# Kernel optimization log

Measured on AMD Instinct MI355X. Metric: run time of the kernel, lower is better.

The kernel has to match this reference:

```python
import jax, jax.numpy as jnp
import numpy as np

D_MODEL = 512
D_PROJ = 32
N_CENT = 6
CORR_HIDDEN = max(D_MODEL // 16, 32)  # 32
LN_EPS = 1e-5
ALPHA_DIR = 5.0


def _layernorm(x, g, b):
    mu = x.mean(axis=-1, keepdims=True)
    var = jnp.mean((x - mu) ** 2, axis=-1, keepdims=True)
    return (x - mu) * jax.lax.rsqrt(var + LN_EPS) * g + b


def _l2norm(x, eps=1e-12):
    n = jnp.sqrt(jnp.sum(x * x, axis=-1, keepdims=True))
    return x / jnp.maximum(n, eps)


def setup_inputs() -> dict:
    key = jax.random.key(0)
    ks = jax.random.split(key, 8)
    B, N = 64, 1024
    x = jax.random.normal(ks[0], (B, N, D_MODEL), dtype=jnp.float32)
    s_in = 1.0 / np.sqrt(D_MODEL)
    proj_w = jax.random.uniform(ks[1], (D_PROJ, D_MODEL), jnp.float32, -s_in, s_in)
    proj_b = jax.random.uniform(ks[2], (D_PROJ,), jnp.float32, -s_in, s_in)
    ln_g = jnp.ones((D_PROJ,), jnp.float32)
    ln_b = jnp.zeros((D_PROJ,), jnp.float32)
    centroids = jax.random.uniform(ks[3], (N_CENT, D_PROJ), jnp.float32, -3.0, 3.0)
    s_c = 1.0 / np.sqrt(D_MODEL + D_PROJ)
    corr_in_w = jax.random.uniform(ks[4], (CORR_HIDDEN, D_MODEL + D_PROJ), jnp.float32, -s_c, s_c)
    corr_in_b = jax.random.uniform(ks[5], (CORR_HIDDEN,), jnp.float32, -s_c, s_c)
    # correction_out is zero-init in the module; use small random values so the
    # correction path is numerically exercised by the baseline.
    corr_out_w = jax.random.normal(ks[6], (D_MODEL, CORR_HIDDEN), jnp.float32) * 0.02
    corr_out_b = jax.random.normal(ks[7], (D_MODEL,), jnp.float32) * 0.02
    return {
        "x": x, "proj_w": proj_w, "proj_b": proj_b, "ln_g": ln_g, "ln_b": ln_b,
        "centroids": centroids,
        "corr_in_w": corr_in_w, "corr_in_b": corr_in_b,
        "corr_out_w": corr_out_w, "corr_out_b": corr_out_b,
        "gate_alpha": jnp.float32(0.0),
        "routing_log_temp": jnp.float32(1.6),
        "scale_evidence": jnp.float32(5.0),
    }


def reference(x, proj_w, proj_b, ln_g, ln_b, centroids, corr_in_w, corr_in_b,
              corr_out_w, corr_out_b, gate_alpha, routing_log_temp, scale_evidence):
    B, N, D = x.shape
    # per-variate RevIN-style normalization over the variate axis (dim=1), unbiased std
    rev_mean = x.mean(axis=1, keepdims=True)
    rev_var = jnp.sum((x - rev_mean) ** 2, axis=1, keepdims=True) / (N - 1)
    rev_std = jnp.sqrt(rev_var) + 1e-5
    x_norm = (x - rev_mean) / rev_std
    # geometric routing: proj -> LN -> cosine sim against centroids
    Q = _layernorm(jnp.einsum("bnd,pd->bnp", x_norm, proj_w) + proj_b, ln_g, ln_b)
    Q_n = _l2norm(Q)                      # [B,N,P]
    K_n = _l2norm(centroids)              # [K,P]
    sim_cos = jnp.einsum("bnp,kp->bnk", Q_n, K_n)
    soft_assign = jax.nn.softmax(sim_cos * jnp.exp(routing_log_temp), axis=-1)
    centroid_ctx = jnp.einsum("bnk,kp->bnp", soft_assign, centroids)
    # centroid-conditioned correction MLP (dropout is identity in eval)
    corr_input = jnp.concatenate([x_norm, centroid_ctx], axis=-1)  # [B,N,D+P]
    h = jax.nn.gelu(jnp.einsum("bnc,hc->bnh", corr_input, corr_in_w) + corr_in_b, approximate=False)
    correction = (jnp.einsum("bnh,dh->bnd", h, corr_out_w) + corr_out_b) * rev_std
    gate = jax.nn.sigmoid(gate_alpha)
    out = x + gate * correction
    # DST uncertainty (no-grad diagnostic)
    sim_ctrl = jax.lax.stop_gradient(sim_cos)
    dir_gate = jax.nn.softplus((sim_ctrl - sim_ctrl.mean(axis=-1, keepdims=True)) * ALPHA_DIR)
    s_ev = jax.nn.softplus(jax.lax.stop_gradient(scale_evidence))
    S_train = jnp.sum(dir_gate * s_ev + 1.0, axis=-1, keepdims=True)
    u_std = N_CENT / S_train
    # losses
    gram = K_n @ K_n.T
    ortho_loss = jnp.mean((gram - jnp.eye(N_CENT, dtype=x.dtype)) ** 2)
    avg_routing = soft_assign.mean(axis=(0, 1))
    latent_loss = jnp.mean((avg_routing - 1.0 / N_CENT) ** 2)
    return out, u_std, ortho_loss, latent_loss
```

## Files before the change

### kernel.cpp

```cpp
#include <hip/hip_runtime.h>
#include <cstdint>
#include <cstddef>

#define N_DIM 1024
#define D_DIM 512
#define M_DIM 65536
#define NC 6

typedef float f32x4 __attribute__((ext_vector_type(4)));
typedef __bf16 bf16x8 __attribute__((ext_vector_type(8)));

__device__ __forceinline__ float sp_f(float z) {
    return z > 20.f ? z : log1pf(expf(z));
}

__global__ void k_pack(const float* __restrict__ pw, const float* __restrict__ ciw,
                       const float* __restrict__ cow, const float* __restrict__ cent,
                       const float* __restrict__ ga, const float* __restrict__ rlt,
                       const float* __restrict__ sev,
                       __bf16* __restrict__ bpa, __bf16* __restrict__ bpl,
                       __bf16* __restrict__ w3p,
                       float* __restrict__ kn, float* __restrict__ cw,
                       float* __restrict__ scal) {
    int bid = blockIdx.x, tid = threadIdx.x;
    if (bid < 128) {
        int i = bid * 256 + tid;
        int c = i >> 9, k = i & 511;
        float w = (c < 32) ? pw[c * 512 + k] : ciw[(c - 32) * 544 + k];
        __bf16 hi = (__bf16)w;
        bpa[i] = hi;
        if (c < 32) bpl[i] = (__bf16)(w - (float)hi);
    } else if (bid < 192) {
        int j = (bid - 128) * 256 + tid;
        w3p[j] = (__bf16)cow[j];
    } else {
        if (tid < 192) {
            int k = tid >> 5, h = tid & 31;
            float s = 0.f;
            for (int p = 0; p < 32; ++p) s += cent[k * 32 + p] * ciw[h * 544 + 512 + p];
            cw[k * 32 + h] = s;
        } else if (tid < 192 + NC) {
            int k = tid - 192;
            float s = 0.f;
            for (int p = 0; p < 32; ++p) { float v = cent[k * 32 + p]; s += v * v; }
            float inv = 1.f / fmaxf(sqrtf(s), 1e-12f);
            for (int p = 0; p < 32; ++p) kn[k * 32 + p] = cent[k * 32 + p] * inv;
        } else if (tid == 198) {
            scal[0] = expf(rlt[0]);
            scal[1] = sp_f(sev[0]);
            scal[2] = 1.f / (1.f + expf(-ga[0]));
        }
    }
}

__global__ void k_ortho(const float* __restrict__ cent, float* __restrict__ out_ortho) {
    __shared__ float skn[NC * 32];
    __shared__ float ssq[36];
    int t = threadIdx.x;
    if (t < NC) {
        float s = 0.f;
        for (int p = 0; p < 32; ++p) { float v = cent[t * 32 + p]; s += v * v; }
        float inv = 1.f / fmaxf(sqrtf(s), 1e-12f);
        for (int p = 0; p < 32; ++p) skn[t * 32 + p] = cent[t * 32 + p] * inv;
    }
    __syncthreads();
    if (t < 36) {
        int i = t / 6, j = t % 6;
        float g = 0.f;
        for (int p = 0; p < 32; ++p) g += skn[i * 32 + p] * skn[j * 32 + p];
        float d = g - (i == j ? 1.f : 0.f);
        ssq[t] = d * d;
    }
    __syncthreads();
    if (t == 0) {
        float s = 0.f;
        for (int i = 0; i < 36; ++i) s += ssq[i];
        *out_ortho = s / 36.f;
    }
}

__global__ void k_stat1(const float* __restrict__ x, float* __restrict__ part) {
    int bid = blockIdx.x;
    int b = bid >> 3, c = bid & 7;
    int d = threadIdx.x;
    const float* px = x + ((size_t)(b * N_DIM + c * 128)) * D_DIM + d;
    float s = 0.f, q = 0.f;
    for (int i = 0; i < 128; ++i) {
        float v = px[(size_t)i * D_DIM];
        s += v; q += v * v;
    }
    size_t o = ((size_t)bid * D_DIM + d) * 2;
    part[o] = s;
    part[o + 1] = q;
}

__global__ void k_stat2(const float* __restrict__ part, float* __restrict__ mean,
                        float* __restrict__ istd, float* __restrict__ stdv) {
    int b = blockIdx.x, d = threadIdx.x;
    float s = 0.f, q = 0.f;
    for (int c = 0; c < 8; ++c) {
        size_t o = (((size_t)(b * 8 + c)) * D_DIM + d) * 2;
        s += part[o]; q += part[o + 1];
    }
    float mu = s * (1.f / (float)N_DIM);
    float var = fmaxf((q - s * mu) * (1.f / (float)(N_DIM - 1)), 0.f);
    float sd = sqrtf(var) + 1e-5f;
    mean[b * D_DIM + d] = mu;
    istd[b * D_DIM + d] = 1.f / sd;
    stdv[b * D_DIM + d] = sd;
}

__launch_bounds__(256)
__global__ void mega(const float* __restrict__ x,
                     const float* __restrict__ proj_b, const float* __restrict__ ln_g,
                     const float* __restrict__ ln_b, const float* __restrict__ cib,
                     const float* __restrict__ cob,
                     const float* __restrict__ mean, const float* __restrict__ istd,
                     const float* __restrict__ stdv,
                     const float* __restrict__ kn, const float* __restrict__ cw,
                     const float* __restrict__ scal,
                     const __bf16* __restrict__ bpa, const __bf16* __restrict__ bpl,
                     const __bf16* __restrict__ w3p,
                     float* __restrict__ out, float* __restrict__ ustd_out,
                     float* __restrict__ rout_part) {
    __shared__ __align__(16) float s_tile[4][16][68];
    __shared__ __align__(16) __bf16 s_h[4][16][40];

    int tid = threadIdx.x;
    int wv = tid >> 6, ln = tid & 63;
    int l15 = ln & 15, lg = ln >> 4;

    int row0 = blockIdx.x * 64;
    int b = row0 >> 10;
    int wrow = row0 + wv * 16;

    const float* xr = x + (size_t)(wrow + l15) * D_DIM;
    const float* mb = mean + b * D_DIM;
    const float* ib = istd + b * D_DIM;

    const __bf16* w0 = bpa + (size_t)l15 * 512;
    const __bf16* w1 = bpa + (size_t)(16 + l15) * 512;
    const __bf16* w2 = bpa + (size_t)(32 + l15) * 512;
    const __bf16* w3 = bpa + (size_t)(48 + l15) * 512;
    const __bf16* wl0 = bpl + (size_t)l15 * 512;
    const __bf16* wl1 = bpl + (size_t)(16 + l15) * 512;

    f32x4 a0 = {0.f, 0.f, 0.f, 0.f}, a1 = a0, a2 = a0, a3 = a0;
    #pragma unroll 4
    for (int ks = 0; ks < 16; ++ks) {
        int k0 = ks * 32 + lg * 8;
        float4 xa = *(const float4*)(xr + k0);
        float4 xb = *(const float4*)(xr + k0 + 4);
        float4 ma = *(const float4*)(mb + k0);
        float4 m2 = *(const float4*)(mb + k0 + 4);
        float4 ia = *(const float4*)(ib + k0);
        float4 i2 = *(const float4*)(ib + k0 + 4);
        float xnf[8];
        xnf[0] = (xa.x - ma.x) * ia.x; xnf[1] = (xa.y - ma.y) * ia.y;
        xnf[2] = (xa.z - ma.z) * ia.z; xnf[3] = (xa.w - ma.w) * ia.w;
        xnf[4] = (xb.x - m2.x) * i2.x; xnf[5] = (xb.y - m2.y) * i2.y;
        xnf[6] = (xb.z - m2.z) * i2.z; xnf[7] = (xb.w - m2.w) * i2.w;
        bf16x8 ah, al;
        #pragma unroll
        for (int j = 0; j < 8; ++j) {
            __bf16 h = (__bf16)xnf[j];
            ah[j] = h;
            al[j] = (__bf16)(xnf[j] - (float)h);
        }
        bf16x8 wh0 = *(const bf16x8*)(w0 + k0);
        bf16x8 wh1 = *(const bf16x8*)(w1 + k0);
        a0 = __builtin_amdgcn_mfma_f32_16x16x32_bf16(ah, wh0, a0, 0, 0, 0);
        a0 = __builtin_amdgcn_mfma_f32_16x16x32_bf16(ah, *(const bf16x8*)(wl0 + k0), a0, 0, 0, 0);
        a0 = __builtin_amdgcn_mfma_f32_16x16x32_bf16(al, wh0, a0, 0, 0, 0);
        a1 = __builtin_amdgcn_mfma_f32_16x16x32_bf16(ah, wh1, a1, 0, 0, 0);
        a1 = __builtin_amdgcn_mfma_f32_16x16x32_bf16(ah, *(const bf16x8*)(wl1 + k0), a1, 0, 0, 0);
        a1 = __builtin_amdgcn_mfma_f32_16x16x32_bf16(al, wh1, a1, 0, 0, 0);
        a2 = __builtin_amdgcn_mfma_f32_16x16x32_bf16(ah, *(const bf16x8*)(w2 + k0), a2, 0, 0, 0);
        a3 = __builtin_amdgcn_mfma_f32_16x16x32_bf16(ah, *(const bf16x8*)(w3 + k0), a3, 0, 0, 0);
    }
    #pragma unroll
    for (int rg = 0; rg < 4; ++rg) {
        s_tile[wv][lg * 4 + rg][l15]      = a0[rg];
        s_tile[wv][lg * 4 + rg][16 + l15] = a1[rg];
        s_tile[wv][lg * 4 + rg][32 + l15] = a2[rg];
        s_tile[wv][lg * 4 + rg][48 + l15] = a3[rg];
    }

    {
        int r = ln >> 2, sub = ln & 3;
        const float* tr = &s_tile[wv][r][0];
        float4 t0 = *(const float4*)(tr + sub * 8);
        float4 t1 = *(const float4*)(tr + sub * 8 + 4);
        float4 pb0 = *(const float4*)(proj_b + sub * 8);
        float4 pb1 = *(const float4*)(proj_b + sub * 8 + 4);
        float P[8];
        P[0] = t0.x + pb0.x; P[1] = t0.y + pb0.y; P[2] = t0.z + pb0.z; P[3] = t0.w + pb0.w;
        P[4] = t1.x + pb1.x; P[5] = t1.y + pb1.y; P[6] = t1.z + pb1.z; P[7] = t1.w + pb1.w;
        float m = 0.f;
        #pragma unroll
        for (int j = 0; j < 8; ++j) m += P[j];
        m += __shfl_xor(m, 1); m += __shfl_xor(m, 2);
        float mu = m * (1.f / 32.f);
        float v = 0.f;
        #pragma unroll
        for (int j = 0; j < 8; ++j) { float d = P[j] - mu; v += d * d; }
        v += __shfl_xor(v, 1); v += __shfl_xor(v, 2);
        float rs = rsqrtf(v * (1.f / 32.f) + 1e-5f);
        float4 g0 = *(const float4*)(ln_g + sub * 8);
        float4 g1 = *(const float4*)(ln_g + sub * 8 + 4);
        float4 bl0 = *(const float4*)(ln_b + sub * 8);
        float4 bl1 = *(const float4*)(ln_b + sub * 8 + 4);
        float gg[8] = {g0.x, g0.y, g0.z, g0.w, g1.x, g1.y, g1.z, g1.w};
        float bb[8] = {bl0.x, bl0.y, bl0.z, bl0.w, bl1.x, bl1.y, bl1.z, bl1.w};
        float q[8]; float n2 = 0.f;
        #pragma unroll
        for (int j = 0; j < 8; ++j) {
            q[j] = (P[j] - mu) * rs * gg[j] + bb[j];
            n2 += q[j] * q[j];
        }
        n2 += __shfl_xor(n2, 1); n2 += __shfl_xor(n2, 2);
        float inv = 1.f / fmaxf(sqrtf(n2), 1e-12f);
        float sim[6];
        #pragma unroll
        for (int k = 0; k < 6; ++k) {
            const float* kr = kn + k * 32 + sub * 8;
            float4 ka = *(const float4*)(kr);
            float4 kb = *(const float4*)(kr + 4);
            float s = q[0] * ka.x + q[1] * ka.y + q[2] * ka.z + q[3] * ka.w
                    + q[4] * kb.x + q[5] * kb.y + q[6] * kb.z + q[7] * kb.w;
            s += __shfl_xor(s, 1); s += __shfl_xor(s, 2);
            sim[k] = s * inv;
        }
        float T = scal[0], sevv = scal[1];
        float mx = sim[0];
        #pragma unroll
        for (int k = 1; k < 6; ++k) mx = fmaxf(mx, sim[k]);
        float e[6], es = 0.f;
        #pragma unroll
        for (int k = 0; k < 6; ++k) { e[k] = expf((sim[k] - mx) * T); es += e[k]; }
        float einv = 1.f / es;
        float a[6];
        #pragma unroll
        for (int k = 0; k < 6; ++k) a[k] = e[k] * einv;
        float msim = 0.f;
        #pragma unroll
        for (int k = 0; k < 6; ++k) msim += sim[k];
        msim *= (1.f / 6.f);
        float S = 6.f;
        #pragma unroll
        for (int k = 0; k < 6; ++k) S += sevv * sp_f((sim[k] - msim) * 5.f);
        if (sub == 0) ustd_out[wrow + r] = 6.f / S;
        float4 h0 = *(const float4*)(tr + 32 + sub * 8);
        float4 h1 = *(const float4*)(tr + 32 + sub * 8 + 4);
        float4 c0 = *(const float4*)(cib + sub * 8);
        float4 c1 = *(const float4*)(cib + sub * 8 + 4);
        float vh[8] = {h0.x + c0.x, h0.y + c0.y, h0.z + c0.z, h0.w + c0.w,
                       h1.x + c1.x, h1.y + c1.y, h1.z + c1.z, h1.w + c1.w};
        #pragma unroll
        for (int k = 0; k < 6; ++k) {
            const float* cr = cw + k * 32 + sub * 8;
            float4 ca = *(const float4*)(cr);
            float4 cb = *(const float4*)(cr + 4);
            vh[0] += a[k] * ca.x; vh[1] += a[k] * ca.y; vh[2] += a[k] * ca.z; vh[3] += a[k] * ca.w;
            vh[4] += a[k] * cb.x; vh[5] += a[k] * cb.y; vh[6] += a[k] * cb.z; vh[7] += a[k] * cb.w;
        }
        bf16x8 hv;
        #pragma unroll
        for (int j = 0; j < 8; ++j) {
            float gv = 0.5f * vh[j] * (1.f + erff(vh[j] * 0.70710678118654752f));
            hv[j] = (__bf16)gv;
        }
        *(bf16x8*)(&s_h[wv][r][sub * 8]) = hv;
        #pragma unroll
        for (int k = 0; k < 6; ++k) {
            float rv = (sub == 0) ? a[k] : 0.f;
            rv += __shfl_xor(rv, 4); rv += __shfl_xor(rv, 8);
            rv += __shfl_xor(rv, 16); rv += __shfl_xor(rv, 32);
            if (ln == 0) atomicAdd(rout_part + (blockIdx.x & 63) * 6 + k, rv);
        }
    }

    bf16x8 ha = *(const bf16x8*)(&s_h[wv][l15][lg * 8]);
    float gate = scal[2];
    const float* sb = stdv + b * D_DIM;
    for (int nf = 0; nf < 32; ++nf) {
        int col = nf * 16 + l15;
        bf16x8 wb = *(const bf16x8*)(w3p + col * 32 + lg * 8);
        f32x4 z = {0.f, 0.f, 0.f, 0.f};
        f32x4 d = __builtin_amdgcn_mfma_f32_16x16x32_bf16(ha, wb, z, 0, 0, 0);
        float bias = cob[col];
        float rsd = sb[col];
        #pragma unroll
        for (int rg = 0; rg < 4; ++rg) {
            size_t idx = (size_t)(wrow + lg * 4 + rg) * D_DIM + col;
            out[idx] = x[idx] + gate * ((d[rg] + bias) * rsd);
        }
    }
}

__global__ void k5(const float* __restrict__ rp, float* __restrict__ out_latent) {
    __shared__ float sv[6];
    int t = threadIdx.x;
    if (t < 6) {
        float s = 0.f;
        for (int i = 0; i < 64; ++i) s += rp[i * 6 + t];
        sv[t] = s;
    }
    __syncthreads();
    if (t == 0) {
        float s = 0.f;
        for (int k = 0; k < 6; ++k) {
            float av = sv[k] * (1.f / (float)M_DIM) - (1.f / 6.f);
            s += av * av;
        }
        *out_latent = s / 6.f;
    }
}

extern "C" void kernel_launch(void* const* d_in, const int* in_sizes, int n_in,
                              void* d_out, int out_size, void* d_ws, size_t ws_size,
                              hipStream_t stream) {
    const float* x      = (const float*)d_in[0];
    const float* proj_w = (const float*)d_in[1];
    const float* proj_b = (const float*)d_in[2];
    const float* ln_g   = (const float*)d_in[3];
    const float* ln_b   = (const float*)d_in[4];
    const float* cent   = (const float*)d_in[5];
    const float* ciw    = (const float*)d_in[6];
    const float* cib    = (const float*)d_in[7];
    const float* cow    = (const float*)d_in[8];
    const float* cob    = (const float*)d_in[9];
    const float* ga     = (const float*)d_in[10];
    const float* rlt    = (const float*)d_in[11];
    const float* sev    = (const float*)d_in[12];

    char* ws = (char*)d_ws;
    float*  rout = (float*)(ws + 0);
    float*  kn   = (float*)(ws + 2048);
    float*  cwv  = (float*)(ws + 4096);
    float*  scal = (float*)(ws + 6144);
    __bf16* bpa  = (__bf16*)(ws + 8192);
    __bf16* bpl  = (__bf16*)(ws + 73728);
    __bf16* w3p  = (__bf16*)(ws + 106496);
    float*  mean = (float*)(ws + 139264);
    float*  istd = (float*)(ws + 270336);
    float*  stdv = (float*)(ws + 401408);

    float* outp   = (float*)d_out;
    float* ustd   = outp + (size_t)M_DIM * D_DIM;
    float* ortho  = ustd + M_DIM;
    float* latent = ortho + 1;

    float* part = (float*)d_out;

    hipMemsetAsync(rout, 0, 64 * 6 * sizeof(float), stream);
    k_pack<<<193, 256, 0, stream>>>(proj_w, ciw, cow, cent, ga, rlt, sev,
                                    bpa, bpl, w3p, kn, cwv, scal);
    k_ortho<<<1, 64, 0, stream>>>(cent, ortho);
    k_stat1<<<512, 512, 0, stream>>>(x, part);
    k_stat2<<<64, 512, 0, stream>>>(part, mean, istd, stdv);
    mega<<<1024, 256, 0, stream>>>(x, proj_b, ln_g, ln_b, cib, cob,
                                   mean, istd, stdv, kn, cwv, scal,
                                   bpa, bpl, w3p, outp, ustd, rout);
    k5<<<1, 64, 0, stream>>>(rout, latent);
}
```

Measured before the change: 146.0 us.

## Split mega kernel K-reduction across wave pairs and vectorize stat pass

The main kernel now gives each 16-row tile to a pair of waves. Each wave in the pair computes half of the 512-wide projection reduction, the partials are summed through shared memory, and the output columns of the correction GEMM are split between the two waves. The grid doubles to 2048 blocks and adds occupancy hints. Per-batch mean, istd, stdv and the output bias are staged once in LDS instead of being read from global memory per lane. The column-statistics kernel uses float4 loads over more, smaller blocks, and the ortho-loss kernel is folded into the pack kernel to save a launch, at the cost of extra block-level synchronisation.

```diff
diff --git a/kernel.cpp b/kernel.cpp
--- a/kernel.cpp
+++ b/kernel.cpp
@@ -21,7 +21,9 @@
                        __bf16* __restrict__ bpa, __bf16* __restrict__ bpl,
                        __bf16* __restrict__ w3p,
                        float* __restrict__ kn, float* __restrict__ cw,
-                       float* __restrict__ scal) {
+                       float* __restrict__ scal, float* __restrict__ out_ortho) {
+    __shared__ float skn[NC * 32];
+    __shared__ float ssq[36];
     int bid = blockIdx.x, tid = threadIdx.x;
     if (bid < 128) {
         int i = bid * 256 + tid;
@@ -33,7 +35,7 @@
     } else if (bid < 192) {
         int j = (bid - 128) * 256 + tid;
         w3p[j] = (__bf16)cow[j];
-    } else {
+    } else if (bid == 192) {
         if (tid < 192) {
             int k = tid >> 5, h = tid & 31;
             float s = 0.f;
@@ -50,57 +52,53 @@
             scal[1] = sp_f(sev[0]);
             scal[2] = 1.f / (1.f + expf(-ga[0]));
         }
-    }
-}
-
-__global__ void k_ortho(const float* __restrict__ cent, float* __restrict__ out_ortho) {
-    __shared__ float skn[NC * 32];
-    __shared__ float ssq[36];
-    int t = threadIdx.x;
-    if (t < NC) {
-        float s = 0.f;
-        for (int p = 0; p < 32; ++p) { float v = cent[t * 32 + p]; s += v * v; }
-        float inv = 1.f / fmaxf(sqrtf(s), 1e-12f);
-        for (int p = 0; p < 32; ++p) skn[t * 32 + p] = cent[t * 32 + p] * inv;
-    }
-    __syncthreads();
-    if (t < 36) {
-        int i = t / 6, j = t % 6;
-        float g = 0.f;
-        for (int p = 0; p < 32; ++p) g += skn[i * 32 + p] * skn[j * 32 + p];
-        float d = g - (i == j ? 1.f : 0.f);
-        ssq[t] = d * d;
-    }
-    __syncthreads();
-    if (t == 0) {
-        float s = 0.f;
-        for (int i = 0; i < 36; ++i) s += ssq[i];
-        *out_ortho = s / 36.f;
+    } else {
+        if (tid < NC) {
+            float s = 0.f;
+            for (int p = 0; p < 32; ++p) { float v = cent[tid * 32 + p]; s += v * v; }
+            float inv = 1.f / fmaxf(sqrtf(s), 1e-12f);
+            for (int p = 0; p < 32; ++p) skn[tid * 32 + p] = cent[tid * 32 + p] * inv;
+        }
+        __syncthreads();
+        if (tid < 36) {
+            int i = tid / 6, j = tid % 6;
+            float g = 0.f;
+            for (int p = 0; p < 32; ++p) g += skn[i * 32 + p] * skn[j * 32 + p];
+            float d = g - (i == j ? 1.f : 0.f);
+            ssq[tid] = d * d;
+        }
+        __syncthreads();
+        if (tid == 0) {
+            float s = 0.f;
+            for (int i = 0; i < 36; ++i) s += ssq[i];
+            *out_ortho = s / 36.f;
+        }
     }
 }
 
 __global__ void k_stat1(const float* __restrict__ x, float* __restrict__ part) {
     int bid = blockIdx.x;
-    int b = bid >> 3, c = bid & 7;
-    int d = threadIdx.x;
-    const float* px = x + ((size_t)(b * N_DIM + c * 128)) * D_DIM + d;
-    float s = 0.f, q = 0.f;
-    for (int i = 0; i < 128; ++i) {
-        float v = px[(size_t)i * D_DIM];
-        s += v; q += v * v;
-    }
-    size_t o = ((size_t)bid * D_DIM + d) * 2;
-    part[o] = s;
-    part[o + 1] = q;
+    int b = bid >> 5, sub = bid & 31;
+    int d4 = threadIdx.x * 4;
+    const float* px = x + ((size_t)(b * 1024 + sub * 32)) * 512 + d4;
+    f32x4 s = {0.f, 0.f, 0.f, 0.f}, q = s;
+    #pragma unroll 4
+    for (int i = 0; i < 32; ++i) {
+        float4 v = *(const float4*)(px + (size_t)i * 512);
+        s.x += v.x; s.y += v.y; s.z += v.z; s.w += v.w;
+        q.x += v.x * v.x; q.y += v.y * v.y; q.z += v.z * v.z; q.w += v.w * v.w;
+    }
+    *(f32x4*)(part + (size_t)bid * 512 + d4) = s;
+    *(f32x4*)(part + (size_t)(2048 + bid) * 512 + d4) = q;
 }
 
 __global__ void k_stat2(const float* __restrict__ part, float* __restrict__ mean,
                         float* __restrict__ istd, float* __restrict__ stdv) {
     int b = blockIdx.x, d = threadIdx.x;
     float s = 0.f, q = 0.f;
-    for (int c = 0; c < 8; ++c) {
-        size_t o = (((size_t)(b * 8 + c)) * D_DIM + d) * 2;
-        s += part[o]; q += part[o + 1];
+    for (int c = 0; c < 32; ++c) {
+        s += part[(size_t)(b * 32 + c) * 512 + d];
+        q += part[(size_t)(2048 + b * 32 + c) * 512 + d];
     }
     float mu = s * (1.f / (float)N_DIM);
     float var = fmaxf((q - s * mu) * (1.f / (float)(N_DIM - 1)), 0.f);
@@ -110,7 +108,7 @@
     stdv[b * D_DIM + d] = sd;
 }
 
-__launch_bounds__(256)
+__launch_bounds__(256, 8)
 __global__ void mega(const float* __restrict__ x,
                      const float* __restrict__ proj_b, const float* __restrict__ ln_g,
                      const float* __restrict__ ln_b, const float* __restrict__ cib,
@@ -123,38 +121,51 @@
                      const __bf16* __restrict__ w3p,
                      float* __restrict__ out, float* __restrict__ ustd_out,
                      float* __restrict__ rout_part) {
-    __shared__ __align__(16) float s_tile[4][16][68];
-    __shared__ __align__(16) __bf16 s_h[4][16][40];
+    __shared__ float s_mean[512];
+    __shared__ float s_is[512];
+    __shared__ float s_sd[512];
+    __shared__ float s_cob[512];
+    __shared__ __align__(16) float s_tile[2][16][68];
+    __shared__ __align__(16) __bf16 s_h[2][16][40];
 
     int tid = threadIdx.x;
     int wv = tid >> 6, ln = tid & 63;
     int l15 = ln & 15, lg = ln >> 4;
-
-    int row0 = blockIdx.x * 64;
-    int b = row0 >> 10;
-    int wrow = row0 + wv * 16;
-
-    const float* xr = x + (size_t)(wrow + l15) * D_DIM;
-    const float* mb = mean + b * D_DIM;
-    const float* ib = istd + b * D_DIM;
-
-    const __bf16* w0 = bpa + (size_t)l15 * 512;
-    const __bf16* w1 = bpa + (size_t)(16 + l15) * 512;
-    const __bf16* w2 = bpa + (size_t)(32 + l15) * 512;
-    const __bf16* w3 = bpa + (size_t)(48 + l15) * 512;
-    const __bf16* wl0 = bpl + (size_t)l15 * 512;
-    const __bf16* wl1 = bpl + (size_t)(16 + l15) * 512;
+    int pair = wv >> 1, h = wv & 1;
+
+    int b = blockIdx.x >> 5;
+    int wrow = blockIdx.x * 32 + pair * 16;
+
+    if (tid < 128) {
+        *(float4*)&s_mean[tid * 4] = *(const float4*)(mean + b * 512 + tid * 4);
+        *(float4*)&s_sd[tid * 4]   = *(const float4*)(stdv + b * 512 + tid * 4);
+    } else {
+        int t = tid - 128;
+        *(float4*)&s_is[t * 4]  = *(const float4*)(istd + b * 512 + t * 4);
+        *(float4*)&s_cob[t * 4] = *(const float4*)(cob + t * 4);
+    }
+    __syncthreads();
+
+    int kbase = h * 256;
+    const float* xr = x + (size_t)(wrow + l15) * 512 + kbase;
+    const __bf16* w0  = bpa + (size_t)l15 * 512 + kbase;
+    const __bf16* w1  = bpa + (size_t)(16 + l15) * 512 + kbase;
+    const __bf16* w2  = bpa + (size_t)(32 + l15) * 512 + kbase;
+    const __bf16* w3  = bpa + (size_t)(48 + l15) * 512 + kbase;
+    const __bf16* wl0 = bpl + (size_t)l15 * 512 + kbase;
+    const __bf16* wl1 = bpl + (size_t)(16 + l15) * 512 + kbase;
 
     f32x4 a0 = {0.f, 0.f, 0.f, 0.f}, a1 = a0, a2 = a0, a3 = a0;
     #pragma unroll 4
-    for (int ks = 0; ks < 16; ++ks) {
+    for (int ks = 0; ks < 8; ++ks) {
         int k0 = ks * 32 + lg * 8;
+        int kk = kbase + k0;
         float4 xa = *(const float4*)(xr + k0);
         float4 xb = *(const float4*)(xr + k0 + 4);
-        float4 ma = *(const float4*)(mb + k0);
-        float4 m2 = *(const float4*)(mb + k0 + 4);
-        float4 ia = *(const float4*)(ib + k0);
-        float4 i2 = *(const float4*)(ib + k0 + 4);
+        float4 ma = *(const float4*)&s_mean[kk];
+        float4 m2 = *(const float4*)&s_mean[kk + 4];
+        float4 ia = *(const float4*)&s_is[kk];
+        float4 i2 = *(const float4*)&s_is[kk + 4];
         float xnf[8];
         xnf[0] = (xa.x - ma.x) * ia.x; xnf[1] = (xa.y - ma.y) * ia.y;
         xnf[2] = (xa.z - ma.z) * ia.z; xnf[3] = (xa.w - ma.w) * ia.w;
@@ -163,9 +174,9 @@
         bf16x8 ah, al;
         #pragma unroll
         for (int j = 0; j < 8; ++j) {
-            __bf16 h = (__bf16)xnf[j];
-            ah[j] = h;
-            al[j] = (__bf16)(xnf[j] - (float)h);
+            __bf16 hh = (__bf16)xnf[j];
+            ah[j] = hh;
+            al[j] = (__bf16)(xnf[j] - (float)hh);
         }
         bf16x8 wh0 = *(const bf16x8*)(w0 + k0);
         bf16x8 wh1 = *(const bf16x8*)(w1 + k0);
@@ -178,17 +189,31 @@
         a2 = __builtin_amdgcn_mfma_f32_16x16x32_bf16(ah, *(const bf16x8*)(w2 + k0), a2, 0, 0, 0);
         a3 = __builtin_amdgcn_mfma_f32_16x16x32_bf16(ah, *(const bf16x8*)(w3 + k0), a3, 0, 0, 0);
     }
-    #pragma unroll
-    for (int rg = 0; rg < 4; ++rg) {
-        s_tile[wv][lg * 4 + rg][l15]      = a0[rg];
-        s_tile[wv][lg * 4 + rg][16 + l15] = a1[rg];
-        s_tile[wv][lg * 4 + rg][32 + l15] = a2[rg];
-        s_tile[wv][lg * 4 + rg][48 + l15] = a3[rg];
-    }
-
-    {
+
+    if (h == 1) {
+        #pragma unroll
+        for (int rg = 0; rg < 4; ++rg) {
+            int row = lg * 4 + rg;
+            s_tile[pair][row][l15]      = a0[rg];
+            s_tile[pair][row][16 + l15] = a1[rg];
+            s_tile[pair][row][32 + l15] = a2[rg];
+            s_tile[pair][row][48 + l15] = a3[rg];
+        }
+    }
+    __syncthreads();
+
+    if (h == 0) {
+        #pragma unroll
+        for (int rg = 0; rg < 4; ++rg) {
+            int row = lg * 4 + rg;
+            s_tile[pair][row][l15]      += a0[rg];
+            s_tile[pair][row][16 + l15] += a1[rg];
+            s_tile[pair][row][32 + l15] += a2[rg];
+            s_tile[pair][row][48 + l15] += a3[rg];
+        }
+
         int r = ln >> 2, sub = ln & 3;
-        const float* tr = &s_tile[wv][r][0];
+        const float* tr = &s_tile[pair][r][0];
         float4 t0 = *(const float4*)(tr + sub * 8);
         float4 t1 = *(const float4*)(tr + sub * 8 + 4);
         float4 pb0 = *(const float4*)(proj_b + sub * 8);
@@ -270,7 +295,7 @@
             float gv = 0.5f * vh[j] * (1.f + erff(vh[j] * 0.70710678118654752f));
             hv[j] = (__bf16)gv;
         }
-        *(bf16x8*)(&s_h[wv][r][sub * 8]) = hv;
+        *(bf16x8*)(&s_h[pair][r][sub * 8]) = hv;
         #pragma unroll
         for (int k = 0; k < 6; ++k) {
             float rv = (sub == 0) ? a[k] : 0.f;
@@ -279,20 +304,21 @@
             if (ln == 0) atomicAdd(rout_part + (blockIdx.x & 63) * 6 + k, rv);
         }
     }
-
-    bf16x8 ha = *(const bf16x8*)(&s_h[wv][l15][lg * 8]);
+    __syncthreads();
+
+    bf16x8 ha = *(const bf16x8*)(&s_h[pair][l15][lg * 8]);
     float gate = scal[2];
-    const float* sb = stdv + b * D_DIM;
-    for (int nf = 0; nf < 32; ++nf) {
+    int nf0 = h * 16;
+    for (int nf = nf0; nf < nf0 + 16; ++nf) {
         int col = nf * 16 + l15;
         bf16x8 wb = *(const bf16x8*)(w3p + col * 32 + lg * 8);
         f32x4 z = {0.f, 0.f, 0.f, 0.f};
         f32x4 d = __builtin_amdgcn_mfma_f32_16x16x32_bf16(ha, wb, z, 0, 0, 0);
-        float bias = cob[col];
-        float rsd = sb[col];
+        float bias = s_cob[col];
+        float rsd = s_sd[col];
         #pragma unroll
         for (int rg = 0; rg < 4; ++rg) {
-            size_t idx = (size_t)(wrow + lg * 4 + rg) * D_DIM + col;
+            size_t idx = (size_t)(wrow + lg * 4 + rg) * 512 + col;
             out[idx] = x[idx] + gate * ((d[rg] + bias) * rsd);
         }
     }
@@ -354,12 +380,11 @@
     float* part = (float*)d_out;
 
     hipMemsetAsync(rout, 0, 64 * 6 * sizeof(float), stream);
-    k_pack<<<193, 256, 0, stream>>>(proj_w, ciw, cow, cent, ga, rlt, sev,
-                                    bpa, bpl, w3p, kn, cwv, scal);
-    k_ortho<<<1, 64, 0, stream>>>(cent, ortho);
-    k_stat1<<<512, 512, 0, stream>>>(x, part);
+    k_pack<<<194, 256, 0, stream>>>(proj_w, ciw, cow, cent, ga, rlt, sev,
+                                    bpa, bpl, w3p, kn, cwv, scal, ortho);
+    k_stat1<<<2048, 128, 0, stream>>>(x, part);
     k_stat2<<<64, 512, 0, stream>>>(part, mean, istd, stdv);
-    mega<<<1024, 256, 0, stream>>>(x, proj_b, ln_g, ln_b, cib, cob,
+    mega<<<2048, 256, 0, stream>>>(x, proj_b, ln_g, ln_b, cib, cob,
                                    mean, istd, stdv, kn, cwv, scal,
                                    bpa, bpl, w3p, outp, ustd, rout);
     k5<<<1, 64, 0, stream>>>(rout, latent);
```

Measured after the change: 193.5 us. +32.5%, slower.
